# Performance work log

Hardware: AMD Instinct MI355X
Metric: run time of the kernel (lower is better)

Reference implementation:

```python
import jax, jax.numpy as jnp
import numpy as np
import math

EMBED_DIM = 512
NUM_HEADS = 8
HEAD_DIM = EMBED_DIM // NUM_HEADS
B, S = 4, 2048


def setup_inputs() -> dict:
    key = jax.random.key(0)
    ks = jax.random.split(key, 12)
    d = EMBED_DIM
    # Xavier-uniform bound for square linear layers
    bound = math.sqrt(6.0 / (d + d))
    def lin_w(k):
        return jax.random.uniform(k, (d, d), jnp.float32, -bound, bound)
    return {
        "x": jax.random.normal(ks[0], (B, S, d), jnp.float32),
        "mask": jax.random.randint(ks[1], (B, S), 0, 2) == 1,  # True = masked out
        "wq": lin_w(ks[2]), "bq": jnp.zeros((d,), jnp.float32),
        "wk": lin_w(ks[3]), "bk": jnp.zeros((d,), jnp.float32),
        "wv": lin_w(ks[4]), "bv": jnp.zeros((d,), jnp.float32),
        "wo": lin_w(ks[5]), "bo": jnp.zeros((d,), jnp.float32),
        "ln_gamma": jnp.ones((d,), jnp.float32),
        "ln_beta": jnp.zeros((d,), jnp.float32),
        "temperature": jnp.full((1,), 1.0 / math.sqrt(HEAD_DIM), jnp.float32),
    }


def _layer_norm(x, gamma, beta, eps=1e-6):
    mu = jnp.mean(x, axis=-1, keepdims=True)
    var = jnp.var(x, axis=-1, keepdims=True)
    return (x - mu) * jax.lax.rsqrt(var + eps) * gamma + beta


def reference(x, mask, wq, bq, wk, bk, wv, bv, wo, bo, ln_gamma, ln_beta, temperature):
    Bv, Sv, d = x.shape
    H, hd = NUM_HEADS, HEAD_DIM
    # torch nn.Linear: y = x @ W.T + b (W is [out, in])
    def proj(w, b):
        return (jnp.einsum("bsd,ed->bse", x, w) + b).reshape(Bv, Sv, H, hd).transpose(0, 2, 1, 3)
    q = proj(wq, bq)  # [B, H, S, hd]
    k = proj(wk, bk)
    v = proj(wv, bv)
    scores = jnp.einsum("bhqd,bhkd->bhqk", q, k) * temperature[0]  # [B,H,S,S]
    scores = jnp.where(mask[:, None, None, :], jnp.float32(-1e9), scores)
    attn = jax.nn.softmax(scores, axis=-1)  # dropout is identity in eval
    out = jnp.einsum("bhqk,bhkd->bhqd", attn, v)
    out = out.transpose(0, 2, 1, 3).reshape(Bv, Sv, d)
    out = jnp.einsum("bsd,ed->bse", out, wo) + bo
    return _layer_norm(out + x, ln_gamma, ln_beta)
```

## Files before the change

kernel.cpp:

```cpp
#include <hip/hip_runtime.h>
#include <hip/hip_bf16.h>
#include <stdint.h>

#define B_ 4
#define S_ 2048
#define D_ 512
#define H_ 8
#define HD_ 64
#define M_ (B_*S_)

typedef __bf16 bf16x8 __attribute__((ext_vector_type(8)));
typedef float f32x4 __attribute__((ext_vector_type(4)));
typedef float f32x16 __attribute__((ext_vector_type(16)));

__device__ __forceinline__ unsigned short f2b(float f) {
  union { float f; unsigned u; } v; v.f = f;
  unsigned r = v.u + 0x7fff + ((v.u >> 16) & 1);
  return (unsigned short)(r >> 16);
}

__device__ __forceinline__ float exp2_hw(float x) {
  return __builtin_amdgcn_exp2f(x);
}

__device__ __forceinline__ unsigned cvtpk_bf16(float lo, float hi) {
  unsigned r;
  asm("v_cvt_pk_bf16_f32 %0, %1, %2" : "=v"(r) : "v"(lo), "v"(hi));
  return r;
}

__device__ __forceinline__ void plswap(unsigned &a, unsigned &b) {
  asm volatile("v_permlane32_swap_b32 %0, %1" : "+v"(a), "+v"(b));
}

__device__ __forceinline__ void gload16(const void* g, void* lds) {
  __builtin_amdgcn_global_load_lds(
      (const __attribute__((address_space(1))) unsigned int*)g,
      (__attribute__((address_space(3))) unsigned int*)lds, 16, 0, 0);
}

#define XN4 (M_ * D_ / 4)
#define WN4 (D_ * D_ / 4)
__global__ __launch_bounds__(256) void cvt_all_kernel(const float* __restrict__ x,
    const float* __restrict__ wq, const float* __restrict__ wk,
    const float* __restrict__ wv, const float* __restrict__ wo,
    unsigned short* __restrict__ xb, unsigned short* __restrict__ wqb,
    unsigned short* __restrict__ wkb, unsigned short* __restrict__ wvb,
    unsigned short* __restrict__ wob) {
  int i = blockIdx.x * blockDim.x + threadIdx.x;
  const float* src; unsigned short* dst; int off;
  if (i < XN4) { src = x; dst = xb; off = i; }
  else {
    int j = i - XN4;
    int sel = j / WN4; off = j - sel * WN4;
    src = (sel == 0) ? wq : (sel == 1) ? wk : (sel == 2) ? wv : wo;
    dst = (sel == 0) ? wqb : (sel == 1) ? wkb : (sel == 2) ? wvb : wob;
  }
  float4 v = ((const float4*)src)[off];
  ushort4 o;
  o.x = f2b(v.x); o.y = f2b(v.y); o.z = f2b(v.z); o.w = f2b(v.w);
  ((ushort4*)dst)[off] = o;
}

__device__ __forceinline__ void gemm_core(const unsigned short* __restrict__ A,
                                          const unsigned short* __restrict__ W,
                                          int m0, int n0, f32x4 (&acc)[4][4],
                                          unsigned short* As, unsigned short* Bs) {
  int tid = threadIdx.x;
  int w = tid >> 6, lane = tid & 63;
  int l15 = lane & 15, g = lane >> 4;
  int wr = w >> 1, wc = w & 1;
  for (int k0 = 0; k0 < D_; k0 += 64) {
    #pragma unroll
    for (int i = 0; i < 4; ++i) {
      int l = i * 256 + w * 64 + lane;
      int row = l >> 3, seg = l & 7;
      int sseg = seg ^ (row & 7);
      gload16(A + (size_t)(m0 + row) * D_ + k0 + sseg * 8,
              (char*)As + (size_t)(i * 256 + w * 64) * 16);
      gload16(W + (size_t)(n0 + row) * D_ + k0 + sseg * 8,
              (char*)Bs + (size_t)(i * 256 + w * 64) * 16);
    }
    __syncthreads();
    #pragma unroll
    for (int kk = 0; kk < 2; ++kk) {
      int sw = ((kk * 4 + g) ^ (l15 & 7)) * 8;
      bf16x8 af[4], bfr[4];
      #pragma unroll
      for (int t = 0; t < 4; ++t) {
        af[t]  = *(const bf16x8*)&As[(wr * 64 + t * 16 + l15) * 64 + sw];
        bfr[t] = *(const bf16x8*)&Bs[(wc * 64 + t * 16 + l15) * 64 + sw];
      }
      #pragma unroll
      for (int mi = 0; mi < 4; ++mi)
        #pragma unroll
        for (int ni = 0; ni < 4; ++ni)
          acc[mi][ni] = __builtin_amdgcn_mfma_f32_16x16x32_bf16(af[mi], bfr[ni], acc[mi][ni], 0, 0, 0);
    }
    __syncthreads();
  }
}

__global__ __launch_bounds__(256) void gemm_qkv(const unsigned short* __restrict__ xb,
    const unsigned short* __restrict__ wqb, const unsigned short* __restrict__ wkb,
    const unsigned short* __restrict__ wvb,
    const float* __restrict__ bq, const float* __restrict__ bk, const float* __restrict__ bv,
    const float* __restrict__ tptr,
    unsigned short* __restrict__ Qb, unsigned short* __restrict__ Kb, unsigned short* __restrict__ Vtb) {
  __shared__ unsigned short As[128 * 64], Bs[128 * 64];
  int z = blockIdx.z;
  const unsigned short* W = (z == 0) ? wqb : ((z == 1) ? wkb : wvb);
  const float* bias = (z == 0) ? bq : ((z == 1) ? bk : bv);
  float scale = (z == 0) ? tptr[0] * 1.44269504088896340736f : 1.0f;
  int m0 = blockIdx.x * 128, n0 = blockIdx.y * 128;
  f32x4 zero4 = {0.f, 0.f, 0.f, 0.f};
  f32x4 acc[4][4];
  #pragma unroll
  for (int mi = 0; mi < 4; ++mi)
    #pragma unroll
    for (int ni = 0; ni < 4; ++ni) acc[mi][ni] = zero4;
  gemm_core(xb, W, m0, n0, acc, As, Bs);
  int tid = threadIdx.x;
  int w = tid >> 6, lane = tid & 63, l15 = lane & 15, g = lane >> 4;
  int wr = w >> 1, wc = w & 1;
  #pragma unroll
  for (int mi = 0; mi < 4; ++mi)
    #pragma unroll
    for (int ni = 0; ni < 4; ++ni) {
      int e = n0 + wc * 64 + ni * 16 + l15;
      float bb = bias[e];
      int h = e >> 6, dd = e & 63;
      #pragma unroll
      for (int r = 0; r < 4; ++r) {
        int m = m0 + wr * 64 + mi * 16 + g * 4 + r;
        int b = m >> 11, s = m & 2047;
        unsigned short u = f2b((acc[mi][ni][r] + bb) * scale);
        int bh = b * H_ + h;
        if (z == 0)      Qb[((size_t)bh * S_ + s) * HD_ + dd] = u;
        else if (z == 1) Kb[((size_t)bh * S_ + s) * HD_ + dd] = u;
        else             Vtb[((size_t)bh * HD_ + dd) * S_ + s] = u;
      }
    }
}

__global__ __launch_bounds__(256) void gemm_proj(const unsigned short* __restrict__ AOb,
    const unsigned short* __restrict__ wob, const float* __restrict__ bo, float* __restrict__ Pf) {
  __shared__ unsigned short As[128 * 64], Bs[128 * 64];
  int m0 = blockIdx.x * 128, n0 = blockIdx.y * 128;
  f32x4 zero4 = {0.f, 0.f, 0.f, 0.f};
  f32x4 acc[4][4];
  #pragma unroll
  for (int mi = 0; mi < 4; ++mi)
    #pragma unroll
    for (int ni = 0; ni < 4; ++ni) acc[mi][ni] = zero4;
  gemm_core(AOb, wob, m0, n0, acc, As, Bs);
  int tid = threadIdx.x;
  int w = tid >> 6, lane = tid & 63, l15 = lane & 15, g = lane >> 4;
  int wr = w >> 1, wc = w & 1;
  #pragma unroll
  for (int mi = 0; mi < 4; ++mi)
    #pragma unroll
    for (int ni = 0; ni < 4; ++ni) {
      int e = n0 + wc * 64 + ni * 16 + l15;
      float bb = bo[e];
      #pragma unroll
      for (int r = 0; r < 4; ++r) {
        int m = m0 + wr * 64 + mi * 16 + g * 4 + r;
        Pf[(size_t)m * D_ + e] = acc[mi][ni][r] + bb;
      }
    }
}

__global__ __launch_bounds__(256, 2) void attn_kernel(const unsigned short* __restrict__ Qb,
    const unsigned short* __restrict__ Kb, const unsigned short* __restrict__ Vtb,
    const int* __restrict__ mask, unsigned short* __restrict__ AOb) {
  __shared__ unsigned short Ks[3][64 * 64], Vs[3][64 * 64];
  __shared__ uint4 mlds[32][4][2];
  int bh = blockIdx.y, b = bh >> 3, h = bh & 7;
  int tid = threadIdx.x, w = tid >> 6, lane = tid & 63;
  int l31 = lane & 31, hi = lane >> 5;
  int q0w = blockIdx.x * 128 + w * 32;
  const unsigned short* Qbase = Qb + (size_t)bh * S_ * HD_;
  const int* mbase = mask + (size_t)b * S_;

  bf16x8 qf[4];
  #pragma unroll
  for (int kk = 0; kk < 4; ++kk)
    qf[kk] = *(const bf16x8*)&Qbase[(size_t)(q0w + l31) * HD_ + kk * 16 + hi * 8];

  bf16x8 ones;
  #pragma unroll
  for (int j = 0; j < 8; ++j) ones[j] = (__bf16)1.0f;

  f32x16 out[2], lacc, zc;
  #pragma unroll
  for (int i = 0; i < 16; ++i) { out[0][i] = 0.f; out[1][i] = 0.f; lacc[i] = 0.f; zc[i] = 0.f; }

  f32x16 stA[2], stB[2];

  #define STAGE_KV(buf, kb_) do {                                              \
    _Pragma("unroll")                                                          \
    for (int i = 0; i < 2; ++i) {                                              \
      int l = i * 256 + w * 64 + lane;                                         \
      int row = l >> 3, seg = l & 7;                                           \
      int sseg = seg ^ (row & 7);                                              \
      gload16(Kb + ((size_t)bh * S_ + (kb_) + row) * HD_ + sseg * 8,           \
              (char*)Ks[buf] + (size_t)(i * 256 + w * 64) * 16);               \
      gload16(Vtb + ((size_t)bh * HD_ + row) * S_ + (kb_) + sseg * 8,          \
              (char*)Vs[buf] + (size_t)(i * 256 + w * 64) * 16);               \
    }                                                                          \
  } while (0)

  #define QKT_TILE(KSBUF, ST) do {                                             \
    __builtin_amdgcn_s_setprio(1);                                             \
    const unsigned short* kbase_ = Ks[KSBUF];                                  \
    _Pragma("unroll")                                                          \
    for (int kk = 0; kk < 4; ++kk) {                                           \
      int sw = ((2 * kk + hi) ^ (l31 & 7)) * 8;                                \
      bf16x8 ka0 = *(const bf16x8*)&kbase_[l31 * 64 + sw];                     \
      bf16x8 ka1 = *(const bf16x8*)&kbase_[(32 + l31) * 64 + sw];              \
      ST[0] = __builtin_amdgcn_mfma_f32_32x32x16_bf16(ka0, qf[kk], kk ? ST[0] : zc, 0, 0, 0); \
      ST[1] = __builtin_amdgcn_mfma_f32_32x32x16_bf16(ka1, qf[kk], kk ? ST[1] : zc, 0, 0, 0); \
    }                                                                          \
    __builtin_amdgcn_s_setprio(0);                                             \
  } while (0)

  #define TILE_BODY(T, STC, STN, bPV, bQK, bST) do {                           \
    __syncthreads();                                                           \
    if ((T) + 2 < 32) STAGE_KV(bST, ((T) + 2) * 64);                           \
    if ((T) + 1 < 32) QKT_TILE(bQK, STN);                                      \
    _Pragma("unroll")                                                          \
    for (int ktile = 0; ktile < 2; ++ktile)                                    \
      _Pragma("unroll")                                                        \
      for (int reg = 0; reg < 16; ++reg)                                       \
        STC[ktile][reg] = exp2_hw(STC[ktile][reg]);                            \
    __builtin_amdgcn_s_setprio(1);                                             \
    const unsigned short* vbase_ = Vs[bPV];                                    \
    _Pragma("unroll")                                                          \
    for (int kp = 0; kp < 4; ++kp) {                                           \
      const int kt8 = kp >> 1;                                                 \
      const int ro = 8 * (kp & 1);                                             \
      uint4 mw = mlds[(T)][kp][hi];                                            \
      unsigned Xa = cvtpk_bf16(STC[kt8][ro + 0], STC[kt8][ro + 1]);            \
      unsigned Ya = cvtpk_bf16(STC[kt8][ro + 4], STC[kt8][ro + 5]);            \
      unsigned Xb = cvtpk_bf16(STC[kt8][ro + 2], STC[kt8][ro + 3]);            \
      unsigned Yb = cvtpk_bf16(STC[kt8][ro + 6], STC[kt8][ro + 7]);            \
      plswap(Xa, Ya);                                                          \
      plswap(Xb, Yb);                                                          \
      union { unsigned u[4]; bf16x8 v; } pu;                                   \
      pu.u[0] = Xa & mw.x; pu.u[1] = Xb & mw.y;                                \
      pu.u[2] = Ya & mw.z; pu.u[3] = Yb & mw.w;                                \
      bf16x8 pa = pu.v;                                                        \
      _Pragma("unroll")                                                        \
      for (int dn = 0; dn < 2; ++dn) {                                         \
        int row = dn * 32 + l31;                                               \
        bf16x8 vb = *(const bf16x8*)&vbase_[row * 64 + ((2 * kp + hi) ^ (row & 7)) * 8]; \
        out[dn] = __builtin_amdgcn_mfma_f32_32x32x16_bf16(pa, vb, out[dn], 0, 0, 0); \
      }                                                                        \
      lacc = __builtin_amdgcn_mfma_f32_32x32x16_bf16(pa, ones, lacc, 0, 0, 0); \
    }                                                                          \
    __builtin_amdgcn_s_setprio(0);                                             \
  } while (0)

  STAGE_KV(0, 0);
  {
    int t = tid;
    int tile = t >> 3, kp = (t >> 1) & 3, hh = t & 1;
    const int* mp = mbase + tile * 64 + kp * 16 + hh * 8;
    uint4 mw;
    mw.x = (mp[0] ? 0u : 0x0000FFFFu) | (mp[1] ? 0u : 0xFFFF0000u);
    mw.y = (mp[2] ? 0u : 0x0000FFFFu) | (mp[3] ? 0u : 0xFFFF0000u);
    mw.z = (mp[4] ? 0u : 0x0000FFFFu) | (mp[5] ? 0u : 0xFFFF0000u);
    mw.w = (mp[6] ? 0u : 0x0000FFFFu) | (mp[7] ? 0u : 0xFFFF0000u);
    mlds[tile][kp][hh] = mw;
  }
  __syncthreads();
  STAGE_KV(1, 64);
  QKT_TILE(0, stA);

  int b0 = 0, b1 = 1, b2 = 2;
  for (int tp = 0; tp < 16; ++tp) {
    int t = 2 * tp;
    TILE_BODY(t, stA, stB, b0, b1, b2);
    TILE_BODY(t + 1, stB, stA, b1, b2, b0);
    int btmp = b0; b0 = b2; b2 = b1; b1 = btmp;
  }

  #pragma unroll
  for (int reg = 0; reg < 16; ++reg) {
    float inv = 1.f / lacc[reg];
    int q = q0w + (reg & 3) + 8 * (reg >> 2) + 4 * hi;
    #pragma unroll
    for (int dn = 0; dn < 2; ++dn)
      AOb[((size_t)b * S_ + q) * D_ + h * HD_ + dn * 32 + l31] = f2b(out[dn][reg] * inv);
  }
  #undef TILE_BODY
  #undef QKT_TILE
  #undef STAGE_KV
}

__global__ __launch_bounds__(256) void ln_kernel(const float* __restrict__ Pf,
    const float* __restrict__ x, const float* __restrict__ gamma,
    const float* __restrict__ beta, float* __restrict__ out) {
  int row = blockIdx.x * 4 + (threadIdx.x >> 6);
  int lane = threadIdx.x & 63;
  const float* pr = Pf + (size_t)row * D_;
  const float* xr = x + (size_t)row * D_;
  float4 a0 = *(const float4*)(pr + lane * 4);
  float4 a1 = *(const float4*)(pr + 256 + lane * 4);
  float4 b0 = *(const float4*)(xr + lane * 4);
  float4 b1 = *(const float4*)(xr + 256 + lane * 4);
  float y[8] = {a0.x + b0.x, a0.y + b0.y, a0.z + b0.z, a0.w + b0.w,
                a1.x + b1.x, a1.y + b1.y, a1.z + b1.z, a1.w + b1.w};
  float s = 0.f, s2 = 0.f;
  #pragma unroll
  for (int i = 0; i < 8; ++i) { s += y[i]; s2 += y[i] * y[i]; }
  #pragma unroll
  for (int d = 1; d < 64; d <<= 1) { s += __shfl_xor(s, d); s2 += __shfl_xor(s2, d); }
  float mu = s * (1.f / 512.f);
  float var = s2 * (1.f / 512.f) - mu * mu;
  float inv = rsqrtf(fmaxf(var, 0.f) + 1e-6f);
  float4 g0 = *(const float4*)(gamma + lane * 4);
  float4 g1 = *(const float4*)(gamma + 256 + lane * 4);
  float4 e0 = *(const float4*)(beta + lane * 4);
  float4 e1 = *(const float4*)(beta + 256 + lane * 4);
  float* orow = out + (size_t)row * D_;
  float4 o0 = {(y[0] - mu) * inv * g0.x + e0.x, (y[1] - mu) * inv * g0.y + e0.y,
               (y[2] - mu) * inv * g0.z + e0.z, (y[3] - mu) * inv * g0.w + e0.w};
  float4 o1 = {(y[4] - mu) * inv * g1.x + e1.x, (y[5] - mu) * inv * g1.y + e1.y,
               (y[6] - mu) * inv * g1.z + e1.z, (y[7] - mu) * inv * g1.w + e1.w};
  *(float4*)(orow + lane * 4) = o0;
  *(float4*)(orow + 256 + lane * 4) = o1;
}

extern "C" void kernel_launch(void* const* d_in, const int* in_sizes, int n_in,
                              void* d_out, int out_size, void* d_ws, size_t ws_size,
                              hipStream_t stream) {
  const float* x = (const float*)d_in[0];
  const int* mask = (const int*)d_in[1];
  const float* wq = (const float*)d_in[2];
  const float* bq = (const float*)d_in[3];
  const float* wk = (const float*)d_in[4];
  const float* bk = (const float*)d_in[5];
  const float* wv = (const float*)d_in[6];
  const float* bv = (const float*)d_in[7];
  const float* wo = (const float*)d_in[8];
  const float* bo = (const float*)d_in[9];
  const float* gamma = (const float*)d_in[10];
  const float* beta = (const float*)d_in[11];
  const float* temp = (const float*)d_in[12];
  float* out = (float*)d_out;
  char* ws = (char*)d_ws;
  const size_t MB = (size_t)1 << 20;
  unsigned short* xb  = (unsigned short*)(ws);
  unsigned short* wqb = (unsigned short*)(ws + 8 * MB);
  unsigned short* wkb = (unsigned short*)(ws + 8 * MB + 512 * 1024);
  unsigned short* wvb = (unsigned short*)(ws + 9 * MB);
  unsigned short* wob = (unsigned short*)(ws + 9 * MB + 512 * 1024);
  unsigned short* Qb  = (unsigned short*)(ws + 10 * MB);
  unsigned short* Kb  = (unsigned short*)(ws + 18 * MB);
  float*          Pf  = (float*)(ws + 10 * MB);
  unsigned short* Vtb = (unsigned short*)(ws + 26 * MB);
  unsigned short* AOb = (unsigned short*)(ws + 34 * MB);

  cvt_all_kernel<<<(XN4 + 4 * WN4 + 255) / 256, 256, 0, stream>>>(
      x, wq, wk, wv, wo, xb, wqb, wkb, wvb, wob);
  gemm_qkv<<<dim3(64, 4, 3), 256, 0, stream>>>(xb, wqb, wkb, wvb, bq, bk, bv, temp, Qb, Kb, Vtb);
  attn_kernel<<<dim3(16, 32), 256, 0, stream>>>(Qb, Kb, Vtb, mask, AOb);
  gemm_proj<<<dim3(64, 4), 256, 0, stream>>>(AOb, wob, bo, Pf);
  ln_kernel<<<2048, 256, 0, stream>>>(Pf, x, gamma, beta, out);
}
```

Measured before the change: 116.7 us.

## Double-buffer GEMM LDS tiles and stage V transpose through shared memory

The GEMM core now keeps two LDS buffers and issues the global-to-LDS loads for the next K slice before computing on the current one, so load latency overlaps with MFMA work. The V projection epilogue writes its tile transposed into a swizzled LDS scratch buffer and then stores 16-byte vectors along the sequence dimension, replacing scattered 2-byte strided writes to Vt. The cost is double the shared memory per block, which may lower occupancy, plus an extra barrier in the V path.

```diff
diff --git a/kernel.cpp b/kernel.cpp
--- a/kernel.cpp
+++ b/kernel.cpp
@@ -62,34 +62,40 @@
   ((ushort4*)dst)[off] = o;
 }
 
-__device__ __forceinline__ void gemm_core(const unsigned short* __restrict__ A,
-                                          const unsigned short* __restrict__ W,
-                                          int m0, int n0, f32x4 (&acc)[4][4],
-                                          unsigned short* As, unsigned short* Bs) {
+__device__ __forceinline__ void gemm_core_db(const unsigned short* __restrict__ A,
+                                             const unsigned short* __restrict__ W,
+                                             int m0, int n0, f32x4 (&acc)[4][4],
+                                             unsigned short (&As)[2][128 * 64],
+                                             unsigned short (&Bs)[2][128 * 64]) {
   int tid = threadIdx.x;
   int w = tid >> 6, lane = tid & 63;
   int l15 = lane & 15, g = lane >> 4;
   int wr = w >> 1, wc = w & 1;
-  for (int k0 = 0; k0 < D_; k0 += 64) {
-    #pragma unroll
-    for (int i = 0; i < 4; ++i) {
-      int l = i * 256 + w * 64 + lane;
-      int row = l >> 3, seg = l & 7;
-      int sseg = seg ^ (row & 7);
-      gload16(A + (size_t)(m0 + row) * D_ + k0 + sseg * 8,
-              (char*)As + (size_t)(i * 256 + w * 64) * 16);
-      gload16(W + (size_t)(n0 + row) * D_ + k0 + sseg * 8,
-              (char*)Bs + (size_t)(i * 256 + w * 64) * 16);
-    }
-    __syncthreads();
+  #define STAGE_G(buf, k0_) do {                                               \
+    _Pragma("unroll")                                                          \
+    for (int i = 0; i < 4; ++i) {                                              \
+      int l = i * 256 + w * 64 + lane;                                         \
+      int row = l >> 3, seg = l & 7;                                           \
+      int sseg = seg ^ (row & 7);                                              \
+      gload16(A + (size_t)(m0 + row) * D_ + (k0_) + sseg * 8,                  \
+              (char*)As[buf] + (size_t)(i * 256 + w * 64) * 16);               \
+      gload16(W + (size_t)(n0 + row) * D_ + (k0_) + sseg * 8,                  \
+              (char*)Bs[buf] + (size_t)(i * 256 + w * 64) * 16);               \
+    }                                                                          \
+  } while (0)
+  STAGE_G(0, 0);
+  __syncthreads();
+  for (int ks = 0; ks < 8; ++ks) {
+    int cur = ks & 1;
+    if (ks < 7) STAGE_G(cur ^ 1, (ks + 1) * 64);
     #pragma unroll
     for (int kk = 0; kk < 2; ++kk) {
       int sw = ((kk * 4 + g) ^ (l15 & 7)) * 8;
       bf16x8 af[4], bfr[4];
       #pragma unroll
       for (int t = 0; t < 4; ++t) {
-        af[t]  = *(const bf16x8*)&As[(wr * 64 + t * 16 + l15) * 64 + sw];
-        bfr[t] = *(const bf16x8*)&Bs[(wc * 64 + t * 16 + l15) * 64 + sw];
+        af[t]  = *(const bf16x8*)&As[cur][(wr * 64 + t * 16 + l15) * 64 + sw];
+        bfr[t] = *(const bf16x8*)&Bs[cur][(wc * 64 + t * 16 + l15) * 64 + sw];
       }
       #pragma unroll
       for (int mi = 0; mi < 4; ++mi)
@@ -99,6 +105,7 @@
     }
     __syncthreads();
   }
+  #undef STAGE_G
 }
 
 __global__ __launch_bounds__(256) void gemm_qkv(const unsigned short* __restrict__ xb,
@@ -107,7 +114,7 @@
     const float* __restrict__ bq, const float* __restrict__ bk, const float* __restrict__ bv,
     const float* __restrict__ tptr,
     unsigned short* __restrict__ Qb, unsigned short* __restrict__ Kb, unsigned short* __restrict__ Vtb) {
-  __shared__ unsigned short As[128 * 64], Bs[128 * 64];
+  __shared__ unsigned short As[2][128 * 64], Bs[2][128 * 64];
   int z = blockIdx.z;
   const unsigned short* W = (z == 0) ? wqb : ((z == 1) ? wkb : wvb);
   const float* bias = (z == 0) ? bq : ((z == 1) ? bk : bv);
@@ -119,33 +126,62 @@
   for (int mi = 0; mi < 4; ++mi)
     #pragma unroll
     for (int ni = 0; ni < 4; ++ni) acc[mi][ni] = zero4;
-  gemm_core(xb, W, m0, n0, acc, As, Bs);
+  gemm_core_db(xb, W, m0, n0, acc, As, Bs);
   int tid = threadIdx.x;
   int w = tid >> 6, lane = tid & 63, l15 = lane & 15, g = lane >> 4;
   int wr = w >> 1, wc = w & 1;
-  #pragma unroll
-  for (int mi = 0; mi < 4; ++mi)
-    #pragma unroll
-    for (int ni = 0; ni < 4; ++ni) {
-      int e = n0 + wc * 64 + ni * 16 + l15;
-      float bb = bias[e];
-      int h = e >> 6, dd = e & 63;
+  if (z == 2) {
+    unsigned short* T = &As[0][0];
+    #pragma unroll
+    for (int mi = 0; mi < 4; ++mi)
       #pragma unroll
-      for (int r = 0; r < 4; ++r) {
-        int m = m0 + wr * 64 + mi * 16 + g * 4 + r;
-        int b = m >> 11, s = m & 2047;
-        unsigned short u = f2b((acc[mi][ni][r] + bb) * scale);
-        int bh = b * H_ + h;
-        if (z == 0)      Qb[((size_t)bh * S_ + s) * HD_ + dd] = u;
-        else if (z == 1) Kb[((size_t)bh * S_ + s) * HD_ + dd] = u;
-        else             Vtb[((size_t)bh * HD_ + dd) * S_ + s] = u;
+      for (int ni = 0; ni < 4; ++ni) {
+        int el = wc * 64 + ni * 16 + l15;
+        float bb = bias[n0 + el];
+        int sx = (el & 15) << 3;
+        #pragma unroll
+        for (int r = 0; r < 4; ++r) {
+          int s = wr * 64 + mi * 16 + g * 4 + r;
+          T[el * 128 + (s ^ sx)] = f2b(acc[mi][ni][r] + bb);
+        }
       }
+    __syncthreads();
+    int el = tid >> 1, hf = tid & 1;
+    int eg = n0 + el, h = eg >> 6, dd = eg & 63;
+    int bI = m0 >> 11, sbase = (m0 & 2047) + hf * 64;
+    unsigned short* dst = &Vtb[((size_t)(bI * H_ + h) * HD_ + dd) * S_ + sbase];
+    const unsigned short* srcR = &T[el * 128];
+    int j = el & 15;
+    #pragma unroll
+    for (int c = 0; c < 8; ++c) {
+      int cc = (hf * 8 + c) ^ j;
+      uint4 v = *(const uint4*)&srcR[cc * 8];
+      *(uint4*)&dst[c * 8] = v;
     }
+  } else {
+    #pragma unroll
+    for (int mi = 0; mi < 4; ++mi)
+      #pragma unroll
+      for (int ni = 0; ni < 4; ++ni) {
+        int e = n0 + wc * 64 + ni * 16 + l15;
+        float bb = bias[e];
+        int h = e >> 6, dd = e & 63;
+        #pragma unroll
+        for (int r = 0; r < 4; ++r) {
+          int m = m0 + wr * 64 + mi * 16 + g * 4 + r;
+          int b = m >> 11, s = m & 2047;
+          unsigned short u = f2b((acc[mi][ni][r] + bb) * scale);
+          int bh = b * H_ + h;
+          if (z == 0) Qb[((size_t)bh * S_ + s) * HD_ + dd] = u;
+          else        Kb[((size_t)bh * S_ + s) * HD_ + dd] = u;
+        }
+      }
+  }
 }
 
 __global__ __launch_bounds__(256) void gemm_proj(const unsigned short* __restrict__ AOb,
     const unsigned short* __restrict__ wob, const float* __restrict__ bo, float* __restrict__ Pf) {
-  __shared__ unsigned short As[128 * 64], Bs[128 * 64];
+  __shared__ unsigned short As[2][128 * 64], Bs[2][128 * 64];
   int m0 = blockIdx.x * 128, n0 = blockIdx.y * 128;
   f32x4 zero4 = {0.f, 0.f, 0.f, 0.f};
   f32x4 acc[4][4];
@@ -153,7 +189,7 @@
   for (int mi = 0; mi < 4; ++mi)
     #pragma unroll
     for (int ni = 0; ni < 4; ++ni) acc[mi][ni] = zero4;
-  gemm_core(AOb, wob, m0, n0, acc, As, Bs);
+  gemm_core_db(AOb, wob, m0, n0, acc, As, Bs);
   int tid = threadIdx.x;
   int w = tid >> 6, lane = tid & 63, l15 = lane & 15, g = lane >> 4;
   int wr = w >> 1, wc = w & 1;
```

Measured after the change: 105.2 us. -9.9%, faster.
